# Optimization experiments

Hardware: AMD Instinct MI355X
Metric: run time of the kernel (lower is better)

Reference implementation:

```python
import jax, jax.numpy as jnp
import numpy as np


def setup_inputs() -> dict:
    key = jax.random.key(0)
    ks = jax.random.split(key, 12)
    B, S, D = 2, 1024, 1024       # batch, seq_len, hidden
    DF_S, DF_E, E = 2048, 512, 8   # shared ffn, expert ffn, n_experts
    W = 0.02                       # weight init scale
    x = jax.random.normal(ks[0], (B, S, D), jnp.float32)
    router_weight = jax.random.normal(ks[1], (E, D), jnp.float32) * W
    sh_gate_w = jax.random.normal(ks[2], (DF_S, D), jnp.float32) * W
    sh_up_w = jax.random.normal(ks[3], (DF_S, D), jnp.float32) * W
    sh_down_w = jax.random.normal(ks[4], (D, DF_S), jnp.float32) * W
    gate_q = jax.random.randint(ks[5], (E, DF_E, D), -128, 128, jnp.int32)
    up_q = jax.random.randint(ks[6], (E, DF_E, D), -128, 128, jnp.int32)
    down_q = jax.random.randint(ks[7], (E, D, DF_E), -128, 128, jnp.int32)
    gate_s = jax.random.uniform(ks[8], (E, DF_E), jnp.float32) * 0.001
    up_s = jax.random.uniform(ks[9], (E, DF_E), jnp.float32) * 0.001
    down_s = jax.random.uniform(ks[10], (E, D), jnp.float32) * 0.001
    alpha = 0.5 + jax.random.uniform(ks[11], (E,), jnp.float32)  # effective_alpha per expert
    return dict(x=x, router_weight=router_weight, sh_gate_w=sh_gate_w,
                sh_up_w=sh_up_w, sh_down_w=sh_down_w, gate_s=gate_s,
                up_s=up_s, down_s=down_s, alpha=alpha, gate_q=gate_q,
                up_q=up_q, down_q=down_q, top_k=2)


def reference(x, router_weight, sh_gate_w, sh_up_w, sh_down_w,
              gate_s, up_s, down_s, alpha, gate_q, up_q, down_q, top_k):
    B, S, D = x.shape
    T = B * S
    E = router_weight.shape[0]
    xf = x.reshape(T, D).astype(jnp.float32)
    # shared SwiGLU MLP
    shared = (jax.nn.silu(xf @ sh_gate_w.T) * (xf @ sh_up_w.T)) @ sh_down_w.T  # [T, D]
    # router: top-k + softmax over selected logits
    logits = xf @ router_weight.T                                # [T, E]
    k = min(int(top_k), E)
    vals, idx = jax.lax.top_k(logits, k)
    w = jax.nn.softmax(vals, axis=-1)                            # [T, k]
    # scatter routing weights into dense combine matrix [T, E] (topk idx are distinct)
    combine = jnp.zeros((T, E), jnp.float32).at[jnp.arange(T)[:, None], idx].add(w)
    # on-the-fly dequantization: int8-range quants * per-row scale
    gw = gate_q.astype(jnp.float32) * gate_s[..., None]          # [E, DF_E, D]
    uw = up_q.astype(jnp.float32) * up_s[..., None]              # [E, DF_E, D]
    dw = down_q.astype(jnp.float32) * down_s[..., None]          # [E, D, DF_E]
    # expert SwiGLU for every (token, expert) pair, combined by routing weights
    g = jnp.einsum('td,efd->tef', xf, gw)                        # [T, E, DF_E]
    u = jnp.einsum('td,efd->tef', xf, uw)
    eo = jnp.einsum('tef,edf->ted', jax.nn.silu(g) * u, dw)      # [T, E, D]
    delta = eo - shared[:, None, :]                              # expert output minus shared
    mixed = shared + jnp.einsum('te,ted->td', combine * alpha[None, :], delta)
    return mixed.reshape(B, S, D)
```

## Files before the change

### kernel.cpp

```cpp
#include <hip/hip_runtime.h>
#include <math.h>

#define T_TOK 2048
#define D_DIM 1024
#define E_NUM 8
#define DFS   2048
#define DFE   512

#define BK 32

typedef short short8 __attribute__((ext_vector_type(8)));
typedef float floatx4 __attribute__((ext_vector_type(4)));
typedef unsigned short ushort;

__device__ __forceinline__ ushort f2b(float f) {
  union { float f; unsigned u; } v; v.f = f;
  unsigned r = (v.u + 0x7fffu + ((v.u >> 16) & 1u)) >> 16;
  return (ushort)r;
}

__device__ __forceinline__ void gld16(const ushort* g, ushort* l) {
  __builtin_amdgcn_global_load_lds(
      (const __attribute__((address_space(1))) void*)g,
      (__attribute__((address_space(3))) void*)l,
      16, 0, 0);
}

__device__ __forceinline__ float silu_mul(float g, float u) {
  return (g / (1.f + __expf(-g))) * u;
}

__global__ __launch_bounds__(256) void mega_prep(
    const float* __restrict__ x, const float* __restrict__ rw,
    const float* __restrict__ alpha,
    const float* __restrict__ sg, const float* __restrict__ su,
    const float* __restrict__ sd,
    const int* __restrict__ gq, const int* __restrict__ uq,
    const int* __restrict__ dq,
    int* __restrict__ choice, float2* __restrict__ cpair,
    float* __restrict__ csum, ushort* __restrict__ xb,
    ushort* __restrict__ sgb, ushort* __restrict__ subb,
    ushort* __restrict__ sdb,
    ushort* __restrict__ gqb, ushort* __restrict__ uqb,
    ushort* __restrict__ dqb) {
  const int b = blockIdx.x;
  const int tid = threadIdx.x;
  if (b < 512) {
    __shared__ float xs[4 * D_DIM];
    const size_t base = (size_t)b * 4 * D_DIM;
#pragma unroll
    for (int j = 0; j < 4; ++j) {
      const int idx = j * 1024 + tid * 4;
      float4 v = *(const float4*)(x + base + idx);
      *(float4*)&xs[idx] = v;
      union { ushort u[4]; uint2 p; } o;
      o.u[0] = f2b(v.x); o.u[1] = f2b(v.y); o.u[2] = f2b(v.z); o.u[3] = f2b(v.w);
      *(uint2*)(xb + base + idx) = o.p;
    }
    __syncthreads();
    const int w = tid >> 6, l = tid & 63;
    const int t = b * 4 + w;
    const int e = l >> 3, sub = l & 7;
    const float* wr = rw + e * D_DIM;
    float acc = 0.f;
#pragma unroll
    for (int k = 0; k < 32; ++k) {
      const int d = k * 32 + sub * 4;
      float4 xv = *(const float4*)&xs[w * D_DIM + d];
      float4 wv = *(const float4*)(wr + d);
      acc += xv.x * wv.x + xv.y * wv.y + xv.z * wv.z + xv.w * wv.w;
    }
    acc += __shfl_xor(acc, 1);
    acc += __shfl_xor(acc, 2);
    acc += __shfl_xor(acc, 4);
    float lg[8];
#pragma unroll
    for (int i = 0; i < 8; ++i) lg[i] = __shfl(acc, i * 8);
    if (l == 0) {
      int i0 = 0; float v0 = lg[0];
#pragma unroll
      for (int i = 1; i < E_NUM; ++i) if (lg[i] > v0) { v0 = lg[i]; i0 = i; }
      int i1 = -1; float v1 = -1e30f;
#pragma unroll
      for (int i = 0; i < E_NUM; ++i) {
        if (i == i0) continue;
        if (lg[i] > v1) { v1 = lg[i]; i1 = i; }
      }
      float w0 = 1.f / (1.f + __expf(v1 - v0));
      float w1 = 1.f - w0;
      float c0 = w0 * alpha[i0];
      float c1 = w1 * alpha[i1];
      csum[t] = c0 + c1;
      choice[t] = i0 | (i1 << 4);
      cpair[t] = make_float2(c0, c1);
    }
  } else if (b < 512 + 3072) {
    const int bb = b - 512;
    const int which = bb >> 10;
    const float* src; ushort* dst;
    if (which == 0) { src = sg; dst = sgb; }
    else if (which == 1) { src = su; dst = subb; }
    else { src = sd; dst = sdb; }
    const size_t i = (size_t)(bb & 1023) * 256 + tid;
    const float4* sp = (const float4*)src;
    float4 a = sp[2 * i], c = sp[2 * i + 1];
    union { ushort u[8]; uint4 v; } o;
    o.u[0] = f2b(a.x); o.u[1] = f2b(a.y); o.u[2] = f2b(a.z); o.u[3] = f2b(a.w);
    o.u[4] = f2b(c.x); o.u[5] = f2b(c.y); o.u[6] = f2b(c.z); o.u[7] = f2b(c.w);
    ((uint4*)dst)[i] = o.v;
  } else {
    const int bb = b - 3584;
    const int which = bb >> 11;
    const int* src; ushort* dst;
    if (which == 0) { src = gq; dst = gqb; }
    else if (which == 1) { src = uq; dst = uqb; }
    else { src = dq; dst = dqb; }
    const size_t i = (size_t)(bb & 2047) * 256 + tid;
    const int4* sp = (const int4*)src;
    int4 a = sp[2 * i], c = sp[2 * i + 1];
    union { ushort u[8]; uint4 v; } o;
    o.u[0] = f2b((float)a.x); o.u[1] = f2b((float)a.y);
    o.u[2] = f2b((float)a.z); o.u[3] = f2b((float)a.w);
    o.u[4] = f2b((float)c.x); o.u[5] = f2b((float)c.y);
    o.u[6] = f2b((float)c.z); o.u[7] = f2b((float)c.w);
    ((uint4*)dst)[i] = o.v;
  }
}

__global__ __launch_bounds__(1024) void build_lists(
    const int* __restrict__ choice, int* __restrict__ cnt,
    int* __restrict__ tok_list, uint2* __restrict__ ass) {
  __shared__ int lcnt[E_NUM];
  __shared__ int lbase[E_NUM];
  const int tid = threadIdx.x;
  if (tid < E_NUM) lcnt[tid] = 0;
  __syncthreads();
  uint2 tmp[T_TOK / 1024];
#pragma unroll
  for (int r = 0; r < T_TOK / 1024; ++r) {
    const int t = r * 1024 + tid;
    const int ch = choice[t];
    const int i0 = ch & 15, i1 = ch >> 4;
    const int p0 = atomicAdd(&lcnt[i0], 1);
    tok_list[i0 * T_TOK + p0] = t;
    const int p1 = atomicAdd(&lcnt[i1], 1);
    tok_list[i1 * T_TOK + p1] = t;
    tmp[r] = make_uint2((unsigned)((i0 << 16) | p0), (unsigned)((i1 << 16) | p1));
  }
  __syncthreads();
  if (tid < E_NUM) {
    int b = 0;
    for (int i = 0; i < tid; ++i) b += lcnt[i];
    lbase[tid] = b;
    cnt[tid] = lcnt[tid];
    cnt[8 + tid] = b;
  }
  __syncthreads();
#pragma unroll
  for (int r = 0; r < T_TOK / 1024; ++r) {
    const int t = r * 1024 + tid;
    const uint2 v = tmp[r];
    ass[t] = make_uint2(lbase[v.x >> 16] + (v.x & 0xffffu),
                        lbase[v.y >> 16] + (v.y & 0xffffu));
  }
}

#define SZGU (256 * BK)

__global__ __launch_bounds__(256) void mfma_gateup_all(
    const ushort* __restrict__ xb,
    const ushort* __restrict__ wg, const ushort* __restrict__ wu,
    const ushort* __restrict__ gq, const ushort* __restrict__ uq,
    const float* __restrict__ gate_s, const float* __restrict__ up_s,
    const int* __restrict__ cnt, const int* __restrict__ tok_list,
    ushort* __restrict__ sbuf, ushort* __restrict__ act) {
  const int bid = blockIdx.x;
  const bool is_sh = (bid < 512);
  const int tid = threadIdx.x;
  const int wave = tid >> 6, lane = tid & 63;
  const int wr = wave >> 1, wc = wave & 1;
  const int srow = lane >> 2;
  const int scol = (((lane & 3) ^ ((lane >> 3) & 3)) * 8);
  const int K = D_DIM;

  int m0, n0, e = 0, ce = 0, ebase = 0;
  const ushort *aR0, *aR1, *g0, *u0;
  if (is_sh) {
    n0 = (bid & 31) * 64;
    m0 = (bid >> 5) * 128;
    aR0 = xb + (size_t)(m0 + wave * 16 + srow) * K + scol;
    aR1 = aR0 + (size_t)64 * K;
    g0 = wg + (size_t)(n0 + wave * 16 + srow) * K + scol;
    u0 = wu + (size_t)(n0 + wave * 16 + srow) * K + scol;
  } else {
    const int r = bid - 512;
    e = r & 7;
    const int rr = r >> 3;
    n0 = (rr & 7) * 64;
    m0 = (rr >> 3) * 128;
    ce = cnt[e];
    if (m0 >= ce) return;
    ebase = cnt[8 + e];
    const int r0 = m0 + wave * 16 + srow;
    const int r1 = r0 + 64;
    const int tk0 = (r0 < ce) ? tok_list[e * T_TOK + r0] : 0;
    const int tk1 = (r1 < ce) ? tok_list[e * T_TOK + r1] : 0;
    aR0 = xb + (size_t)tk0 * K + scol;
    aR1 = xb + (size_t)tk1 * K + scol;
    g0 = gq + (size_t)e * DFE * D_DIM + (size_t)(n0 + wave * 16 + srow) * K + scol;
    u0 = uq + (size_t)e * DFE * D_DIM + (size_t)(n0 + wave * 16 + srow) * K + scol;
  }

  __shared__ ushort L[3 * SZGU];
  const int woff = (wave * 16) * BK;

  floatx4 accg[4][2], accu[4][2];
#pragma unroll
  for (int i = 0; i < 4; ++i)
#pragma unroll
    for (int j = 0; j < 2; ++j) { accg[i][j] = (floatx4)(0.f); accu[i][j] = (floatx4)(0.f); }

  const int kc = (((lane >> 4) ^ ((lane >> 1) & 3)) * 8);
  const int rb = lane & 15;
  const ushort* dA = &L[(wr * 64 + rb) * BK + kc];
  const ushort* dG = &L[128 * BK + (wc * 32 + rb) * BK + kc];
  const ushort* dU = &L[192 * BK + (wc * 32 + rb) * BK + kc];

#define STAGE_GU(bu, kk)                                        \
  do {                                                          \
    gld16(aR0 + (kk) * BK, &L[(bu) * SZGU] + woff);             \
    gld16(aR1 + (kk) * BK, &L[(bu) * SZGU] + 64 * BK + woff);   \
    gld16(g0 + (kk) * BK, &L[(bu) * SZGU] + 128 * BK + woff);   \
    gld16(u0 + (kk) * BK, &L[(bu) * SZGU] + 192 * BK + woff);   \
  } while (0)

  const int NK = K / BK;
  STAGE_GU(0, 0);
  STAGE_GU(1, 1);

#pragma unroll
  for (int k = 0; k < NK; ++k) {
    if (k < NK - 1) {
      asm volatile("s_waitcnt vmcnt(4)" ::: "memory");
    } else {
      asm volatile("s_waitcnt vmcnt(0)" ::: "memory");
    }
    __builtin_amdgcn_s_barrier();
    asm volatile("" ::: "memory");
    const int bo = (k % 3) * SZGU;
    short8 af[4], gf[2], uf[2];
#pragma unroll
    for (int mt = 0; mt < 4; ++mt)
      af[mt] = *(const short8*)&dA[bo + mt * 16 * BK];
#pragma unroll
    for (int nt = 0; nt < 2; ++nt) {
      gf[nt] = *(const short8*)&dG[bo + nt * 16 * BK];
      uf[nt] = *(const short8*)&dU[bo + nt * 16 * BK];
    }
    if (k + 2 < NK) STAGE_GU((k + 2) % 3, k + 2);
    __builtin_amdgcn_s_setprio(1);
#pragma unroll
    for (int mt = 0; mt < 4; ++mt)
#pragma unroll
      for (int nt = 0; nt < 2; ++nt) {
        accg[mt][nt] = __builtin_amdgcn_mfma_f32_16x16x32_bf16(af[mt], gf[nt], accg[mt][nt], 0, 0, 0);
        accu[mt][nt] = __builtin_amdgcn_mfma_f32_16x16x32_bf16(af[mt], uf[nt], accu[mt][nt], 0, 0, 0);
      }
    __builtin_amdgcn_s_setprio(0);
    asm volatile("s_waitcnt lgkmcnt(0)" ::: "memory");
  }
#undef STAGE_GU

  if (is_sh) {
#pragma unroll
    for (int mt = 0; mt < 4; ++mt)
#pragma unroll
      for (int nt = 0; nt < 2; ++nt) {
        const int col = n0 + wc * 32 + nt * 16 + rb;
#pragma unroll
        for (int r = 0; r < 4; ++r) {
          const int row = m0 + wr * 64 + mt * 16 + (lane >> 4) * 4 + r;
          float s = silu_mul(accg[mt][nt][r], accu[mt][nt][r]);
          sbuf[(size_t)row * DFS + col] = f2b(s);
        }
      }
  } else {
#pragma unroll
    for (int mt = 0; mt < 4; ++mt)
#pragma unroll
      for (int nt = 0; nt < 2; ++nt) {
        const int col = n0 + wc * 32 + nt * 16 + rb;
        const float gsc = gate_s[e * DFE + col];
        const float usc = up_s[e * DFE + col];
#pragma unroll
        for (int r = 0; r < 4; ++r) {
          const int slot = m0 + wr * 64 + mt * 16 + (lane >> 4) * 4 + r;
          if (slot < ce) {
            float s = silu_mul(accg[mt][nt][r] * gsc, accu[mt][nt][r] * usc);
            act[(size_t)(ebase + slot) * DFE + col] = f2b(s);
          }
        }
      }
  }
}

#define SZDN (256 * BK)

__global__ __launch_bounds__(256) void mfma_down_all(
    const ushort* __restrict__ sb, const ushort* __restrict__ wd,
    const ushort* __restrict__ act, const ushort* __restrict__ dq,
    const float* __restrict__ down_s, const int* __restrict__ cnt,
    float* __restrict__ shd0, float* __restrict__ shd1,
    float* __restrict__ pbuf) {
  const int bid = blockIdx.x;
  const bool is_sh = (bid < 256);
  const int tid = threadIdx.x;
  const int wave = tid >> 6, lane = tid & 63;
  const int wr = wave >> 1, wc = wave & 1;
  const int srow = lane >> 2;
  const int scol = (((lane & 3) ^ ((lane >> 3) & 3)) * 8);

  int m0, n0, e = 0, ce = 0, ebase = 0;
  const ushort *aR0, *aR1, *bR0, *bR1;
  float* dst;
  if (is_sh) {
    const int z = bid >> 7;
    const int rr = bid & 127;
    n0 = (rr & 7) * 128;
    m0 = (rr >> 3) * 128;
    const int kb = z * (DFS / 2);
    dst = z ? shd1 : shd0;
    aR0 = sb + (size_t)(m0 + wave * 16 + srow) * DFS + kb + scol;
    aR1 = aR0 + (size_t)64 * DFS;
    bR0 = wd + (size_t)(n0 + wave * 16 + srow) * DFS + kb + scol;
    bR1 = bR0 + (size_t)64 * DFS;
  } else {
    const int r = bid - 256;
    e = r & 7;
    const int rr = r >> 3;
    n0 = (rr & 7) * 128;
    m0 = (rr >> 3) * 128;
    ce = cnt[e];
    if (m0 >= ce) return;
    ebase = cnt[8 + e];
    dst = pbuf;
    aR0 = act + (size_t)(ebase + m0 + wave * 16 + srow) * DFE + scol;
    aR1 = aR0 + (size_t)64 * DFE;
    bR0 = dq + (size_t)e * D_DIM * DFE + (size_t)(n0 + wave * 16 + srow) * DFE + scol;
    bR1 = bR0 + (size_t)64 * DFE;
  }

  __shared__ ushort L[3 * SZDN];
  const int woff = (wave * 16) * BK;

  floatx4 acc[4][4];
#pragma unroll
  for (int i = 0; i < 4; ++i)
#pragma unroll
    for (int j = 0; j < 4; ++j) acc[i][j] = (floatx4)(0.f);

  const int kc = (((lane >> 4) ^ ((lane >> 1) & 3)) * 8);
  const int rb = lane & 15;
  const ushort* dA = &L[(wr * 64 + rb) * BK + kc];
  const ushort* dB = &L[128 * BK + (wc * 64 + rb) * BK + kc];

#define STAGE_DN(bu, kk)                                        \
  do {                                                          \
    gld16(aR0 + (kk) * BK, &L[(bu) * SZDN] + woff);             \
    gld16(aR1 + (kk) * BK, &L[(bu) * SZDN] + 64 * BK + woff);   \
    gld16(bR0 + (kk) * BK, &L[(bu) * SZDN] + 128 * BK + woff);  \
    gld16(bR1 + (kk) * BK, &L[(bu) * SZDN] + 192 * BK + woff);  \
  } while (0)

#define DOWN_LOOP(NKC)                                                        \
  do {                                                                        \
    STAGE_DN(0, 0);                                                           \
    STAGE_DN(1, 1);                                                           \
    _Pragma("unroll")                                                         \
    for (int k = 0; k < (NKC); ++k) {                                         \
      if (k < (NKC) - 1) {                                                    \
        asm volatile("s_waitcnt vmcnt(4)" ::: "memory");                      \
      } else {                                                                \
        asm volatile("s_waitcnt vmcnt(0)" ::: "memory");                      \
      }                                                                       \
      __builtin_amdgcn_s_barrier();                                           \
      asm volatile("" ::: "memory");                                          \
      const int bo = (k % 3) * SZDN;                                          \
      short8 af[4], bf[4];                                                    \
      _Pragma("unroll")                                                       \
      for (int mt = 0; mt < 4; ++mt)                                          \
        af[mt] = *(const short8*)&dA[bo + mt * 16 * BK];                      \
      _Pragma("unroll")                                                       \
      for (int nt = 0; nt < 4; ++nt)                                          \
        bf[nt] = *(const short8*)&dB[bo + nt * 16 * BK];                      \
      if (k + 2 < (NKC)) STAGE_DN((k + 2) % 3, k + 2);                        \
      __builtin_amdgcn_s_setprio(1);                                          \
      _Pragma("unroll")                                                       \
      for (int mt = 0; mt < 4; ++mt)                                          \
        _Pragma("unroll")                                                     \
        for (int nt = 0; nt < 4; ++nt)                                        \
          acc[mt][nt] = __builtin_amdgcn_mfma_f32_16x16x32_bf16(af[mt], bf[nt], acc[mt][nt], 0, 0, 0); \
      __builtin_amdgcn_s_setprio(0);                                          \
      asm volatile("s_waitcnt lgkmcnt(0)" ::: "memory");                      \
    }                                                                         \
  } while (0)

  if (is_sh) {
    DOWN_LOOP(DFS / 2 / BK);
  } else {
    DOWN_LOOP(DFE / BK);
  }
#undef DOWN_LOOP
#undef STAGE_DN

  if (is_sh) {
#pragma unroll
    for (int mt = 0; mt < 4; ++mt)
#pragma unroll
      for (int nt = 0; nt < 4; ++nt) {
        const int col = n0 + wc * 64 + nt * 16 + rb;
#pragma unroll
        for (int r = 0; r < 4; ++r) {
          const int row = m0 + wr * 64 + mt * 16 + (lane >> 4) * 4 + r;
          dst[(size_t)row * D_DIM + col] = acc[mt][nt][r];
        }
      }
  } else {
#pragma unroll
    for (int mt = 0; mt < 4; ++mt)
#pragma unroll
      for (int nt = 0; nt < 4; ++nt) {
        const int col = n0 + wc * 64 + nt * 16 + rb;
        const float dsc = down_s[e * D_DIM + col];
#pragma unroll
        for (int r = 0; r < 4; ++r) {
          const int slot = m0 + wr * 64 + mt * 16 + (lane >> 4) * 4 + r;
          if (slot < ce)
            dst[(size_t)(ebase + slot) * D_DIM + col] = acc[mt][nt][r] * dsc;
        }
      }
  }
}

__global__ __launch_bounds__(256) void combine_kernel(
    const float* __restrict__ shd0, const float* __restrict__ shd1,
    const float* __restrict__ pbuf, const float* __restrict__ csum,
    const float2* __restrict__ cpair, const uint2* __restrict__ ass,
    float* __restrict__ out) {
  const int t = blockIdx.x;
  const int c4 = threadIdx.x * 4;
  const float cs = 1.f - csum[t];
  const float2 cp = cpair[t];
  const uint2 a = ass[t];
  const size_t idx = (size_t)t * D_DIM + c4;
  float4 s0 = *(const float4*)(shd0 + idx);
  float4 s1 = *(const float4*)(shd1 + idx);
  float4 e0 = *(const float4*)(pbuf + (size_t)a.x * D_DIM + c4);
  float4 e1 = *(const float4*)(pbuf + (size_t)a.y * D_DIM + c4);
  float4 o;
  o.x = cs * (s0.x + s1.x) + cp.x * e0.x + cp.y * e1.x;
  o.y = cs * (s0.y + s1.y) + cp.x * e0.y + cp.y * e1.y;
  o.z = cs * (s0.z + s1.z) + cp.x * e0.z + cp.y * e1.z;
  o.w = cs * (s0.w + s1.w) + cp.x * e0.w + cp.y * e1.w;
  *(float4*)(out + idx) = o;
}

extern "C" void kernel_launch(void* const* d_in, const int* in_sizes, int n_in,
                              void* d_out, int out_size, void* d_ws, size_t ws_size,
                              hipStream_t stream) {
  const float* x         = (const float*)d_in[0];
  const float* rw        = (const float*)d_in[1];
  const float* sh_gate_w = (const float*)d_in[2];
  const float* sh_up_w   = (const float*)d_in[3];
  const float* sh_down_w = (const float*)d_in[4];
  const float* gate_s    = (const float*)d_in[5];
  const float* up_s      = (const float*)d_in[6];
  const float* down_s    = (const float*)d_in[7];
  const float* alpha     = (const float*)d_in[8];
  const int*   gate_q    = (const int*)d_in[9];
  const int*   up_q      = (const int*)d_in[10];
  const int*   down_q    = (const int*)d_in[11];

  char* ws = (char*)d_ws;
  const size_t MB = 1u << 20;
  int*    cnt      = (int*)ws;
  int*    tok_list = (int*)(ws + 1024);
  float*  csum     = (float*)(ws + 66560);
  int*    choice   = (int*)(ws + 74752);
  float2* cpair    = (float2*)(ws + 82944);
  uint2*  ass      = (uint2*)(ws + 99328);
  ushort* xb      = (ushort*)(ws + 1 * MB);
  ushort* sgb     = (ushort*)(ws + 5 * MB);
  ushort* sub     = (ushort*)(ws + 9 * MB);
  float*  shd0    = (float*)(ws + 5 * MB);
  ushort* sbuf    = (ushort*)(ws + 13 * MB);
  ushort* sdb     = (ushort*)(ws + 21 * MB);
  ushort* gqb     = (ushort*)(ws + 25 * MB);
  ushort* uqb     = (ushort*)(ws + 33 * MB);
  float*  pbuf    = (float*)(ws + 25 * MB);
  ushort* dqb     = (ushort*)(ws + 41 * MB);
  ushort* act     = (ushort*)(ws + 49 * MB);
  float*  shd1    = (float*)(ws + 53 * MB);

  float* out = (float*)d_out;

  mega_prep<<<9728, 256, 0, stream>>>(
      x, rw, alpha, sh_gate_w, sh_up_w, sh_down_w, gate_q, up_q, down_q,
      choice, cpair, csum, xb, sgb, sub, sdb, gqb, uqb, dqb);
  build_lists<<<1, 1024, 0, stream>>>(choice, cnt, tok_list, ass);

  mfma_gateup_all<<<512 + 1024, 256, 0, stream>>>(
      xb, sgb, sub, gqb, uqb, gate_s, up_s, cnt, tok_list, sbuf, act);
  mfma_down_all<<<256 + 1024, 256, 0, stream>>>(
      sbuf, sdb, act, dqb, down_s, cnt, shd0, shd1, pbuf);
  combine_kernel<<<T_TOK, 256, 0, stream>>>(shd0, shd1, pbuf, csum, cpair, ass, out);
}
```

Measured before the change: 212.0 us.

## Switch GEMM pipelines to double-buffered 64-wide K stages with fewer barriers

Result: no change. 214.2 us (+1.0%).

```diff
diff --git a/kernel.cpp b/kernel.cpp
--- a/kernel.cpp
+++ b/kernel.cpp
@@ -165,7 +165,7 @@
   }
 }
 
-#define SZGU (256 * BK)
+#define SZH (256 * BK)
 
 __global__ __launch_bounds__(256) void mfma_gateup_all(
     const ushort* __restrict__ xb,
@@ -211,7 +211,7 @@
     u0 = uq + (size_t)e * DFE * D_DIM + (size_t)(n0 + wave * 16 + srow) * K + scol;
   }
 
-  __shared__ ushort L[3 * SZGU];
+  __shared__ ushort L[4 * SZH];
   const int woff = (wave * 16) * BK;
 
   floatx4 accg[4][2], accu[4][2];
@@ -226,50 +226,73 @@
   const ushort* dG = &L[128 * BK + (wc * 32 + rb) * BK + kc];
   const ushort* dU = &L[192 * BK + (wc * 32 + rb) * BK + kc];
 
-#define STAGE_GU(bu, kk)                                        \
-  do {                                                          \
-    gld16(aR0 + (kk) * BK, &L[(bu) * SZGU] + woff);             \
-    gld16(aR1 + (kk) * BK, &L[(bu) * SZGU] + 64 * BK + woff);   \
-    gld16(g0 + (kk) * BK, &L[(bu) * SZGU] + 128 * BK + woff);   \
-    gld16(u0 + (kk) * BK, &L[(bu) * SZGU] + 192 * BK + woff);   \
+#define STAGE64(bu, kk)                                               \
+  do {                                                                \
+    ushort* B_ = &L[(bu) * 2 * SZH];                                  \
+    gld16(aR0 + (kk) * 64, B_ + woff);                                \
+    gld16(aR1 + (kk) * 64, B_ + 64 * BK + woff);                      \
+    gld16(g0 + (kk) * 64, B_ + 128 * BK + woff);                      \
+    gld16(u0 + (kk) * 64, B_ + 192 * BK + woff);                      \
+    gld16(aR0 + (kk) * 64 + 32, B_ + SZH + woff);                     \
+    gld16(aR1 + (kk) * 64 + 32, B_ + SZH + 64 * BK + woff);           \
+    gld16(g0 + (kk) * 64 + 32, B_ + SZH + 128 * BK + woff);           \
+    gld16(u0 + (kk) * 64 + 32, B_ + SZH + 192 * BK + woff);           \
   } while (0)
 
-  const int NK = K / BK;
-  STAGE_GU(0, 0);
-  STAGE_GU(1, 1);
-
-#pragma unroll
-  for (int k = 0; k < NK; ++k) {
-    if (k < NK - 1) {
-      asm volatile("s_waitcnt vmcnt(4)" ::: "memory");
-    } else {
-      asm volatile("s_waitcnt vmcnt(0)" ::: "memory");
-    }
+  const int NK2 = K / 64;
+  STAGE64(0, 0);
+
+#pragma unroll
+  for (int k = 0; k < NK2; ++k) {
+    asm volatile("s_waitcnt vmcnt(0)" ::: "memory");
     __builtin_amdgcn_s_barrier();
     asm volatile("" ::: "memory");
-    const int bo = (k % 3) * SZGU;
-    short8 af[4], gf[2], uf[2];
-#pragma unroll
-    for (int mt = 0; mt < 4; ++mt)
-      af[mt] = *(const short8*)&dA[bo + mt * 16 * BK];
-#pragma unroll
-    for (int nt = 0; nt < 2; ++nt) {
-      gf[nt] = *(const short8*)&dG[bo + nt * 16 * BK];
-      uf[nt] = *(const short8*)&dU[bo + nt * 16 * BK];
+    const int bo = (k & 1) * 2 * SZH;
+    {
+      short8 af[4], gf[2], uf[2];
+#pragma unroll
+      for (int mt = 0; mt < 4; ++mt)
+        af[mt] = *(const short8*)&dA[bo + mt * 16 * BK];
+#pragma unroll
+      for (int nt = 0; nt < 2; ++nt) {
+        gf[nt] = *(const short8*)&dG[bo + nt * 16 * BK];
+        uf[nt] = *(const short8*)&dU[bo + nt * 16 * BK];
+      }
+      if (k + 1 < NK2) STAGE64((k + 1) & 1, k + 1);
+      __builtin_amdgcn_s_setprio(1);
+#pragma unroll
+      for (int mt = 0; mt < 4; ++mt)
+#pragma unroll
+        for (int nt = 0; nt < 2; ++nt) {
+          accg[mt][nt] = __builtin_amdgcn_mfma_f32_16x16x32_bf16(af[mt], gf[nt], accg[mt][nt], 0, 0, 0);
+          accu[mt][nt] = __builtin_amdgcn_mfma_f32_16x16x32_bf16(af[mt], uf[nt], accu[mt][nt], 0, 0, 0);
+        }
+      __builtin_amdgcn_s_setprio(0);
     }
-    if (k + 2 < NK) STAGE_GU((k + 2) % 3, k + 2);
-    __builtin_amdgcn_s_setprio(1);
-#pragma unroll
-    for (int mt = 0; mt < 4; ++mt)
+    {
+      short8 af[4], gf[2], uf[2];
+      const int b1 = bo + SZH;
+#pragma unroll
+      for (int mt = 0; mt < 4; ++mt)
+        af[mt] = *(const short8*)&dA[b1 + mt * 16 * BK];
 #pragma unroll
       for (int nt = 0; nt < 2; ++nt) {
-        accg[mt][nt] = __builtin_amdgcn_mfma_f32_16x16x32_bf16(af[mt], gf[nt], accg[mt][nt], 0, 0, 0);
-        accu[mt][nt] = __builtin_amdgcn_mfma_f32_16x16x32_bf16(af[mt], uf[nt], accu[mt][nt], 0, 0, 0);
-      }
-    __builtin_amdgcn_s_setprio(0);
+        gf[nt] = *(const short8*)&dG[b1 + nt * 16 * BK];
+        uf[nt] = *(const short8*)&dU[b1 + nt * 16 * BK];
+      }
+      __builtin_amdgcn_s_setprio(1);
+#pragma unroll
+      for (int mt = 0; mt < 4; ++mt)
+#pragma unroll
+        for (int nt = 0; nt < 2; ++nt) {
+          accg[mt][nt] = __builtin_amdgcn_mfma_f32_16x16x32_bf16(af[mt], gf[nt], accg[mt][nt], 0, 0, 0);
+          accu[mt][nt] = __builtin_amdgcn_mfma_f32_16x16x32_bf16(af[mt], uf[nt], accu[mt][nt], 0, 0, 0);
+        }
+      __builtin_amdgcn_s_setprio(0);
+    }
     asm volatile("s_waitcnt lgkmcnt(0)" ::: "memory");
   }
-#undef STAGE_GU
+#undef STAGE64
 
   if (is_sh) {
 #pragma unroll
@@ -303,8 +326,6 @@
       }
   }
 }
-
-#define SZDN (256 * BK)
 
 __global__ __launch_bounds__(256) void mfma_down_all(
     const ushort* __restrict__ sb, const ushort* __restrict__ wd,
@@ -350,7 +371,7 @@
     bR1 = bR0 + (size_t)64 * DFE;
   }
 
-  __shared__ ushort L[3 * SZDN];
+  __shared__ ushort L[4 * SZH];
   const int woff = (wave * 16) * BK;
 
   floatx4 acc[4][4];
@@ -364,54 +385,76 @@
   const ushort* dA = &L[(wr * 64 + rb) * BK + kc];
   const ushort* dB = &L[128 * BK + (wc * 64 + rb) * BK + kc];
 
-#define STAGE_DN(bu, kk)                                        \
-  do {                                                          \
-    gld16(aR0 + (kk) * BK, &L[(bu) * SZDN] + woff);             \
-    gld16(aR1 + (kk) * BK, &L[(bu) * SZDN] + 64 * BK + woff);   \
-    gld16(bR0 + (kk) * BK, &L[(bu) * SZDN] + 128 * BK + woff);  \
-    gld16(bR1 + (kk) * BK, &L[(bu) * SZDN] + 192 * BK + woff);  \
+#define STAGE64D(bu, kk)                                              \
+  do {                                                                \
+    ushort* B_ = &L[(bu) * 2 * SZH];                                  \
+    gld16(aR0 + (kk) * 64, B_ + woff);                                \
+    gld16(aR1 + (kk) * 64, B_ + 64 * BK + woff);                      \
+    gld16(bR0 + (kk) * 64, B_ + 128 * BK + woff);                     \
+    gld16(bR1 + (kk) * 64, B_ + 192 * BK + woff);                     \
+    gld16(aR0 + (kk) * 64 + 32, B_ + SZH + woff);                     \
+    gld16(aR1 + (kk) * 64 + 32, B_ + SZH + 64 * BK + woff);           \
+    gld16(bR0 + (kk) * 64 + 32, B_ + SZH + 128 * BK + woff);          \
+    gld16(bR1 + (kk) * 64 + 32, B_ + SZH + 192 * BK + woff);          \
   } while (0)
 
-#define DOWN_LOOP(NKC)                                                        \
+#define HALF_DN(boff)                                                         \
   do {                                                                        \
-    STAGE_DN(0, 0);                                                           \
-    STAGE_DN(1, 1);                                                           \
+    short8 af[4], bf[4];                                                      \
     _Pragma("unroll")                                                         \
-    for (int k = 0; k < (NKC); ++k) {                                         \
-      if (k < (NKC) - 1) {                                                    \
-        asm volatile("s_waitcnt vmcnt(4)" ::: "memory");                      \
-      } else {                                                                \
-        asm volatile("s_waitcnt vmcnt(0)" ::: "memory");                      \
-      }                                                                       \
+    for (int mt = 0; mt < 4; ++mt)                                            \
+      af[mt] = *(const short8*)&dA[(boff) + mt * 16 * BK];                    \
+    _Pragma("unroll")                                                         \
+    for (int nt = 0; nt < 4; ++nt)                                            \
+      bf[nt] = *(const short8*)&dB[(boff) + nt * 16 * BK];                    \
+    __builtin_amdgcn_s_setprio(1);                                            \
+    _Pragma("unroll")                                                         \
+    for (int mt = 0; mt < 4; ++mt)                                            \
+      _Pragma("unroll")                                                       \
+      for (int nt = 0; nt < 4; ++nt)                                          \
+        acc[mt][nt] = __builtin_amdgcn_mfma_f32_16x16x32_bf16(af[mt], bf[nt], acc[mt][nt], 0, 0, 0); \
+    __builtin_amdgcn_s_setprio(0);                                            \
+  } while (0)
+
+#define DOWN_LOOP(NKC2)                                                       \
+  do {                                                                        \
+    STAGE64D(0, 0);                                                           \
+    _Pragma("unroll")                                                         \
+    for (int k = 0; k < (NKC2); ++k) {                                        \
+      asm volatile("s_waitcnt vmcnt(0)" ::: "memory");                        \
       __builtin_amdgcn_s_barrier();                                           \
       asm volatile("" ::: "memory");                                          \
-      const int bo = (k % 3) * SZDN;                                          \
-      short8 af[4], bf[4];                                                    \
-      _Pragma("unroll")                                                       \
-      for (int mt = 0; mt < 4; ++mt)                                          \
-        af[mt] = *(const short8*)&dA[bo + mt * 16 * BK];                      \
-      _Pragma("unroll")                                                       \
-      for (int nt = 0; nt < 4; ++nt)                                          \
-        bf[nt] = *(const short8*)&dB[bo + nt * 16 * BK];                      \
-      if (k + 2 < (NKC)) STAGE_DN((k + 2) % 3, k + 2);                        \
-      __builtin_amdgcn_s_setprio(1);                                          \
-      _Pragma("unroll")                                                       \
-      for (int mt = 0; mt < 4; ++mt)                                          \
+      const int bo = (k & 1) * 2 * SZH;                                       \
+      {                                                                       \
+        short8 af[4], bf[4];                                                  \
+        _Pragma("unroll")                                                     \
+        for (int mt = 0; mt < 4; ++mt)                                        \
+          af[mt] = *(const short8*)&dA[bo + mt * 16 * BK];                    \
         _Pragma("unroll")                                                     \
         for (int nt = 0; nt < 4; ++nt)                                        \
-          acc[mt][nt] = __builtin_amdgcn_mfma_f32_16x16x32_bf16(af[mt], bf[nt], acc[mt][nt], 0, 0, 0); \
-      __builtin_amdgcn_s_setprio(0);                                          \
+          bf[nt] = *(const short8*)&dB[bo + nt * 16 * BK];                    \
+        if (k + 1 < (NKC2)) STAGE64D((k + 1) & 1, k + 1);                     \
+        __builtin_amdgcn_s_setprio(1);                                        \
+        _Pragma("unroll")                                                     \
+        for (int mt = 0; mt < 4; ++mt)                                        \
+          _Pragma("unroll")                                                   \
+          for (int nt = 0; nt < 4; ++nt)                                      \
+            acc[mt][nt] = __builtin_amdgcn_mfma_f32_16x16x32_bf16(af[mt], bf[nt], acc[mt][nt], 0, 0, 0); \
+        __builtin_amdgcn_s_setprio(0);                                        \
+      }                                                                       \
+      HALF_DN(bo + SZH);                                                      \
       asm volatile("s_waitcnt lgkmcnt(0)" ::: "memory");                      \
     }                                                                         \
   } while (0)
 
   if (is_sh) {
-    DOWN_LOOP(DFS / 2 / BK);
+    DOWN_LOOP(DFS / 2 / 64);
   } else {
-    DOWN_LOOP(DFE / BK);
+    DOWN_LOOP(DFE / 64);
   }
 #undef DOWN_LOOP
-#undef STAGE_DN
+#undef HALF_DN
+#undef STAGE64D
 
   if (is_sh) {
 #pragma unroll
```
